# Optimization experiments

Hardware: AMD Instinct MI355X
Metric: run time of the kernel (lower is better)

The kernel has to match this reference:

```python
import jax, jax.numpy as jnp
import numpy as np

N_NODES = 50000
N_EDGES = 300000
D = 256


def setup_inputs() -> dict:
    key = jax.random.key(0)
    k1, k2, k3, k4, k5 = jax.random.split(key, 5)
    edge_feat = jax.random.normal(k1, (N_EDGES, D), dtype=jnp.float32)
    node_feat = jax.random.normal(k2, (N_NODES, D), dtype=jnp.float32)
    src_idx = jax.random.randint(k3, (N_EDGES,), 0, N_NODES, dtype=jnp.int32)
    tgt_idx = jax.random.randint(k4, (N_EDGES,), 0, N_NODES, dtype=jnp.int32)
    W = jax.random.normal(k5, (3 * D, D), dtype=jnp.float32) * (1.0 / np.sqrt(3 * D))
    b = jnp.zeros((D,), dtype=jnp.float32)
    return {"edge_feat": edge_feat, "node_feat": node_feat,
            "src_idx": src_idx, "tgt_idx": tgt_idx, "W": W, "b": b}


def reference(edge_feat, node_feat, src_idx, tgt_idx, W, b):
    # broadcast_node_to_edges: gather node states for SOURCE and TARGET tags
    src = jnp.take(node_feat, src_idx, axis=0)   # [E, D]
    tgt = jnp.take(node_feat, tgt_idx, axis=0)   # [E, D]
    # NextStateFromConcat: concat edge input + node inputs, then Dense+relu
    x = jnp.concatenate([edge_feat, src, tgt], axis=-1)  # [E, 3D]
    return jax.nn.relu(x @ W + b)                        # [E, D]
```

## Files before the change

kernel.cpp:

```cpp
#include <hip/hip_runtime.h>
#include <hip/hip_bf16.h>

typedef __attribute__((ext_vector_type(8))) short short8;
typedef __attribute__((ext_vector_type(4))) float floatx4;

#define D_DIM 256
#define K_DIM 768
#define BM 64
#define BK 32
#define PAD 40
#define NSTEP 24

__device__ __forceinline__ short f2bf(float x) {
    union { float f; unsigned u; } a; a.f = x;
    unsigned r = a.u + 0x7fffu + ((a.u >> 16) & 1u);
    return (short)(r >> 16);
}

__global__ __launch_bounds__(256) void wt_kernel(const float* __restrict__ W,
                                                 short* __restrict__ Wt) {
    __shared__ float tile[32][33];
    const int k0 = blockIdx.x * 32, n0 = blockIdx.y * 32;
    const int tx = threadIdx.x & 31, ty = threadIdx.x >> 5;
#pragma unroll
    for (int i = 0; i < 32; i += 8)
        tile[ty + i][tx] = W[(size_t)(k0 + ty + i) * D_DIM + n0 + tx];
    __syncthreads();
#pragma unroll
    for (int i = 0; i < 32; i += 8)
        Wt[(size_t)(n0 + ty + i) * K_DIM + k0 + tx] = f2bf(tile[tx][ty + i]);
}

__global__ __launch_bounds__(256, 3) void edge_gemm(
    const float* __restrict__ edge, const float* __restrict__ node,
    const int* __restrict__ src, const int* __restrict__ tgt,
    const short* __restrict__ Wt, const float* __restrict__ bias,
    float* __restrict__ out, int E)
{
    __shared__ short As[2][BM][PAD];
    __shared__ short Bs[2][D_DIM][PAD];

    const int tid = threadIdx.x;
    const int m0 = blockIdx.x * BM;

    const int arow = tid >> 2;
    const int achk = (tid & 3) * 8;
    int rs = m0 + arow; if (rs >= E) rs = E - 1;
    const int si = src[rs], ti = tgt[rs];
    const float* a0 = edge + (size_t)rs * D_DIM + achk;
    const float* a1 = node + (size_t)si * D_DIM + achk;
    const float* a2 = node + (size_t)ti * D_DIM + achk;
    const short* wrow = Wt + (size_t)tid * K_DIM;

    const int lane = tid & 63;
    const int wv = tid >> 6;
    const int fr = lane & 15;
    const int kq = (lane >> 4) * 8;

    floatx4 acc[4][4] = {};

    float4 pA0, pA1, qA0, qA1;
    short8 rB0, rB1, rB2, rB3;

#define LOADA(d0, d1, t) { \
    const int sg_ = (t) >> 3; \
    const float* ab_ = sg_ == 0 ? a0 : (sg_ == 1 ? a1 : a2); \
    const float4* ap_ = (const float4*)(ab_ + ((t) & 7) * BK); \
    d0 = ap_[0]; d1 = ap_[1]; }

#define LOADB(t) { \
    const short8* bp_ = (const short8*)(wrow + (t) * BK); \
    rB0 = bp_[0]; rB1 = bp_[1]; rB2 = bp_[2]; rB3 = bp_[3]; }

#define STORE(b, s0, s1) { \
    union { short8 v; short s[8]; } u_; \
    u_.s[0] = f2bf(s0.x); u_.s[1] = f2bf(s0.y); u_.s[2] = f2bf(s0.z); u_.s[3] = f2bf(s0.w); \
    u_.s[4] = f2bf(s1.x); u_.s[5] = f2bf(s1.y); u_.s[6] = f2bf(s1.z); u_.s[7] = f2bf(s1.w); \
    *(short8*)&As[b][arow][achk] = u_.v; \
    *(short8*)&Bs[b][tid][0]  = rB0; \
    *(short8*)&Bs[b][tid][8]  = rB1; \
    *(short8*)&Bs[b][tid][16] = rB2; \
    *(short8*)&Bs[b][tid][24] = rB3; }

#define COMPUTE(b) { \
    short8 bfr0 = *(const short8*)&Bs[b][wv * 64 +  0 + fr][kq]; \
    short8 bfr1 = *(const short8*)&Bs[b][wv * 64 + 16 + fr][kq]; \
    short8 bfr2 = *(const short8*)&Bs[b][wv * 64 + 32 + fr][kq]; \
    short8 bfr3 = *(const short8*)&Bs[b][wv * 64 + 48 + fr][kq]; \
    _Pragma("unroll") \
    for (int i_ = 0; i_ < 4; ++i_) { \
        short8 afr = *(const short8*)&As[b][i_ * 16 + fr][kq]; \
        acc[i_][0] = __builtin_amdgcn_mfma_f32_16x16x32_bf16(afr, bfr0, acc[i_][0], 0, 0, 0); \
        acc[i_][1] = __builtin_amdgcn_mfma_f32_16x16x32_bf16(afr, bfr1, acc[i_][1], 0, 0, 0); \
        acc[i_][2] = __builtin_amdgcn_mfma_f32_16x16x32_bf16(afr, bfr2, acc[i_][2], 0, 0, 0); \
        acc[i_][3] = __builtin_amdgcn_mfma_f32_16x16x32_bf16(afr, bfr3, acc[i_][3], 0, 0, 0); \
    } }

    LOADB(0);
    LOADA(qA0, qA1, 0);
    STORE(0, qA0, qA1);
    LOADA(qA0, qA1, 1);
    __syncthreads();

#pragma unroll 1
    for (int t = 0; t < 22; t += 2) {
        LOADB(t + 1);
        LOADA(pA0, pA1, t + 2);
        COMPUTE(0);
        STORE(1, qA0, qA1);
        __syncthreads();
        LOADB(t + 2);
        LOADA(qA0, qA1, t + 3);
        COMPUTE(1);
        STORE(0, pA0, pA1);
        __syncthreads();
    }
    LOADB(23);
    COMPUTE(0);
    STORE(1, qA0, qA1);
    __syncthreads();
    COMPUTE(1);

#undef LOADA
#undef LOADB
#undef STORE
#undef COMPUTE

    float bv[4];
#pragma unroll
    for (int j = 0; j < 4; ++j) bv[j] = bias[wv * 64 + j * 16 + fr];
    const int rq = (lane >> 4) * 4;
#pragma unroll
    for (int i = 0; i < 4; ++i) {
        const int rbase = m0 + i * 16 + rq;
#pragma unroll
        for (int j = 0; j < 4; ++j) {
            const int c = wv * 64 + j * 16 + fr;
#pragma unroll
            for (int r = 0; r < 4; ++r) {
                const int rr = rbase + r;
                if (rr < E) {
                    float v = acc[i][j][r] + bv[j];
                    out[(size_t)rr * D_DIM + c] = v > 0.f ? v : 0.f;
                }
            }
        }
    }
}

extern "C" void kernel_launch(void* const* d_in, const int* in_sizes, int n_in,
                              void* d_out, int out_size, void* d_ws, size_t ws_size,
                              hipStream_t stream) {
    const float* edge = (const float*)d_in[0];
    const float* node = (const float*)d_in[1];
    const int*   srcI = (const int*)d_in[2];
    const int*   tgtI = (const int*)d_in[3];
    const float* W    = (const float*)d_in[4];
    const float* bias = (const float*)d_in[5];
    float* out = (float*)d_out;
    const int E = in_sizes[2];
    short* Wt = (short*)d_ws;

    dim3 tgrid(K_DIM / 32, D_DIM / 32);
    wt_kernel<<<tgrid, dim3(256), 0, stream>>>(W, Wt);

    dim3 ggrid((E + BM - 1) / BM);
    edge_gemm<<<ggrid, dim3(256), 0, stream>>>(edge, node, srcI, tgtI, Wt, bias, out, E);
}
```

Measured before the change: 813.6 us.

## Stream weight tiles directly into LDS with pre-swizzled layout

Measured after the change: 661.0 us. 1.23x faster.

```diff
diff --git a/kernel.cpp b/kernel.cpp
--- a/kernel.cpp
+++ b/kernel.cpp
@@ -10,6 +10,7 @@
 #define BK 32
 #define PAD 40
 #define NSTEP 24
+#define BTILE 8192
 
 __device__ __forceinline__ short f2bf(float x) {
     union { float f; unsigned u; } a; a.f = x;
@@ -17,28 +18,27 @@
     return (short)(r >> 16);
 }
 
+__device__ __forceinline__ unsigned swz(unsigned r) {
+    return r ^ (((r >> 7) & 7u) << 4);
+}
+
 __global__ __launch_bounds__(256) void wt_kernel(const float* __restrict__ W,
-                                                 short* __restrict__ Wt) {
-    __shared__ float tile[32][33];
-    const int k0 = blockIdx.x * 32, n0 = blockIdx.y * 32;
-    const int tx = threadIdx.x & 31, ty = threadIdx.x >> 5;
-#pragma unroll
-    for (int i = 0; i < 32; i += 8)
-        tile[ty + i][tx] = W[(size_t)(k0 + ty + i) * D_DIM + n0 + tx];
-    __syncthreads();
-#pragma unroll
-    for (int i = 0; i < 32; i += 8)
-        Wt[(size_t)(n0 + ty + i) * K_DIM + k0 + tx] = f2bf(tile[tx][ty + i]);
+                                                 short* __restrict__ Wt2) {
+    const int k = blockIdx.x;
+    const int n = threadIdx.x;
+    const int t = k >> 5, kk = k & 31;
+    const unsigned r = (unsigned)n * 64u + (unsigned)kk * 2u;
+    Wt2[(size_t)t * BTILE + (swz(r) >> 1)] = f2bf(W[(size_t)k * D_DIM + n]);
 }
 
 __global__ __launch_bounds__(256, 3) void edge_gemm(
     const float* __restrict__ edge, const float* __restrict__ node,
     const int* __restrict__ src, const int* __restrict__ tgt,
-    const short* __restrict__ Wt, const float* __restrict__ bias,
+    const short* __restrict__ Wt2, const float* __restrict__ bias,
     float* __restrict__ out, int E)
 {
-    __shared__ short As[2][BM][PAD];
-    __shared__ short Bs[2][D_DIM][PAD];
+    __shared__ __align__(16) short As[2][BM][PAD];
+    __shared__ __align__(16) short Bs[2][BTILE];
 
     const int tid = threadIdx.x;
     const int m0 = blockIdx.x * BM;
@@ -50,17 +50,36 @@
     const float* a0 = edge + (size_t)rs * D_DIM + achk;
     const float* a1 = node + (size_t)si * D_DIM + achk;
     const float* a2 = node + (size_t)ti * D_DIM + achk;
-    const short* wrow = Wt + (size_t)tid * K_DIM;
 
     const int lane = tid & 63;
     const int wv = tid >> 6;
     const int fr = lane & 15;
     const int kq = (lane >> 4) * 8;
 
+    const char* gb = (const char*)Wt2 + wv * 4096 + lane * 16;
+    char* lb0 = (char*)&Bs[0][0] + wv * 4096;
+    char* lb1 = (char*)&Bs[1][0] + wv * 4096;
+
+    unsigned boff[4];
+#pragma unroll
+    for (int j = 0; j < 4; ++j) {
+        unsigned col = (unsigned)(wv * 64 + j * 16 + fr);
+        boff[j] = swz(col * 64u + (unsigned)(lane >> 4) * 16u);
+    }
+
     floatx4 acc[4][4] = {};
+    float4 pA0, pA1, qA0, qA1;
 
-    float4 pA0, pA1, qA0, qA1;
-    short8 rB0, rB1, rB2, rB3;
+#define GLOADB(t, lb) { \
+    const char* g_ = gb + (size_t)(t) * 16384; \
+    __builtin_amdgcn_global_load_lds((const __attribute__((address_space(1))) unsigned*)(g_), \
+        (__attribute__((address_space(3))) unsigned*)(lb), 16, 0, 0); \
+    __builtin_amdgcn_global_load_lds((const __attribute__((address_space(1))) unsigned*)(g_ + 1024), \
+        (__attribute__((address_space(3))) unsigned*)((lb) + 1024), 16, 0, 0); \
+    __builtin_amdgcn_global_load_lds((const __attribute__((address_space(1))) unsigned*)(g_ + 2048), \
+        (__attribute__((address_space(3))) unsigned*)((lb) + 2048), 16, 0, 0); \
+    __builtin_amdgcn_global_load_lds((const __attribute__((address_space(1))) unsigned*)(g_ + 3072), \
+        (__attribute__((address_space(3))) unsigned*)((lb) + 3072), 16, 0, 0); }
 
 #define LOADA(d0, d1, t) { \
     const int sg_ = (t) >> 3; \
@@ -68,25 +87,18 @@
     const float4* ap_ = (const float4*)(ab_ + ((t) & 7) * BK); \
     d0 = ap_[0]; d1 = ap_[1]; }
 
-#define LOADB(t) { \
-    const short8* bp_ = (const short8*)(wrow + (t) * BK); \
-    rB0 = bp_[0]; rB1 = bp_[1]; rB2 = bp_[2]; rB3 = bp_[3]; }
-
-#define STORE(b, s0, s1) { \
+#define STOREA(b, s0, s1) { \
     union { short8 v; short s[8]; } u_; \
     u_.s[0] = f2bf(s0.x); u_.s[1] = f2bf(s0.y); u_.s[2] = f2bf(s0.z); u_.s[3] = f2bf(s0.w); \
     u_.s[4] = f2bf(s1.x); u_.s[5] = f2bf(s1.y); u_.s[6] = f2bf(s1.z); u_.s[7] = f2bf(s1.w); \
-    *(short8*)&As[b][arow][achk] = u_.v; \
-    *(short8*)&Bs[b][tid][0]  = rB0; \
-    *(short8*)&Bs[b][tid][8]  = rB1; \
-    *(short8*)&Bs[b][tid][16] = rB2; \
-    *(short8*)&Bs[b][tid][24] = rB3; }
+    *(short8*)&As[b][arow][achk] = u_.v; }
 
 #define COMPUTE(b) { \
-    short8 bfr0 = *(const short8*)&Bs[b][wv * 64 +  0 + fr][kq]; \
-    short8 bfr1 = *(const short8*)&Bs[b][wv * 64 + 16 + fr][kq]; \
-    short8 bfr2 = *(const short8*)&Bs[b][wv * 64 + 32 + fr][kq]; \
-    short8 bfr3 = *(const short8*)&Bs[b][wv * 64 + 48 + fr][kq]; \
+    const char* bb_ = (const char*)&Bs[b][0]; \
+    short8 bfr0 = *(const short8*)(bb_ + boff[0]); \
+    short8 bfr1 = *(const short8*)(bb_ + boff[1]); \
+    short8 bfr2 = *(const short8*)(bb_ + boff[2]); \
+    short8 bfr3 = *(const short8*)(bb_ + boff[3]); \
     _Pragma("unroll") \
     for (int i_ = 0; i_ < 4; ++i_) { \
         short8 afr = *(const short8*)&As[b][i_ * 16 + fr][kq]; \
@@ -96,34 +108,34 @@
         acc[i_][3] = __builtin_amdgcn_mfma_f32_16x16x32_bf16(afr, bfr3, acc[i_][3], 0, 0, 0); \
     } }
 
-    LOADB(0);
+    GLOADB(0, lb0);
     LOADA(qA0, qA1, 0);
-    STORE(0, qA0, qA1);
+    STOREA(0, qA0, qA1);
     LOADA(qA0, qA1, 1);
     __syncthreads();
 
 #pragma unroll 1
     for (int t = 0; t < 22; t += 2) {
-        LOADB(t + 1);
+        GLOADB(t + 1, lb1);
         LOADA(pA0, pA1, t + 2);
         COMPUTE(0);
-        STORE(1, qA0, qA1);
+        STOREA(1, qA0, qA1);
         __syncthreads();
-        LOADB(t + 2);
+        GLOADB(t + 2, lb0);
         LOADA(qA0, qA1, t + 3);
         COMPUTE(1);
-        STORE(0, pA0, pA1);
+        STOREA(0, pA0, pA1);
         __syncthreads();
     }
-    LOADB(23);
+    GLOADB(23, lb1);
     COMPUTE(0);
-    STORE(1, qA0, qA1);
+    STOREA(1, qA0, qA1);
     __syncthreads();
     COMPUTE(1);
 
+#undef GLOADB
 #undef LOADA
-#undef LOADB
-#undef STORE
+#undef STOREA
 #undef COMPUTE
 
     float bv[4];
@@ -159,11 +171,10 @@
     const float* bias = (const float*)d_in[5];
     float* out = (float*)d_out;
     const int E = in_sizes[2];
-    short* Wt = (short*)d_ws;
+    short* Wt2 = (short*)d_ws;
 
-    dim3 tgrid(K_DIM / 32, D_DIM / 32);
-    wt_kernel<<<tgrid, dim3(256), 0, stream>>>(W, Wt);
+    wt_kernel<<<dim3(K_DIM), dim3(256), 0, stream>>>(W, Wt2);
 
     dim3 ggrid((E + BM - 1) / BM);
-    edge_gemm<<<ggrid, dim3(256), 0, stream>>>(edge, node, srcI, tgtI, Wt, bias, out, E);
+    edge_gemm<<<ggrid, dim3(256), 0, stream>>>(edge, node, srcI, tgtI, Wt2, bias, out, E);
 }
```
